# Kernel optimization log

Measured on AMD Instinct MI355X. Metric: run time of the kernel, lower is better.

Reference implementation:

```python
import jax, jax.numpy as jnp
import numpy as np

DIM = 768
HEADS = 12
HEAD_DIM = DIM // HEADS  # 64
THETA = 10000.0
B, S = 2, 2048


def rotate_half(x):
    # pairs-interleaved rotate: (x1, x2) -> (-x2, x1)
    xp = x.reshape(x.shape[:-1] + (-1, 2))
    x1, x2 = xp[..., 0], xp[..., 1]
    return jnp.stack((-x2, x1), axis=-1).reshape(x.shape)


def rope_freqs(seq_len, head_dim, dtype):
    inv = 1.0 / (THETA ** (jnp.arange(0, head_dim, 2, dtype=jnp.float32) / head_dim))
    pos = jnp.arange(seq_len, dtype=jnp.float32)
    f = pos[:, None] * inv[None, :]              # [S, head_dim//2]
    f = jnp.repeat(f, 2, axis=-1)                # [S, head_dim]
    return f.astype(dtype)


def apply_rotary(freqs, t):
    # freqs [S, D] broadcasts against t [B, H, S, D]
    return t * jnp.cos(freqs) + rotate_half(t) * jnp.sin(freqs)


def setup_inputs() -> dict:
    key = jax.random.key(0)
    k1, k2, k3 = jax.random.split(key, 3)
    x = jax.random.normal(k1, (B, S, DIM), dtype=jnp.float32)
    W_qkv = jax.random.normal(k2, (3 * DIM, DIM), dtype=jnp.float32) * 0.02
    W_proj = jax.random.normal(k3, (DIM, DIM), dtype=jnp.float32) * 0.02
    b_proj = jnp.zeros((DIM,), dtype=jnp.float32)
    return {"x": x, "W_qkv": W_qkv, "W_proj": W_proj, "b_proj": b_proj}


def reference(x, W_qkv, W_proj, b_proj):
    Bb, Ss, C = x.shape
    qkv = jnp.einsum('bsc,oc->bso', x, W_qkv)                    # [B,S,3C]
    qkv = qkv.reshape(Bb, Ss, 3, HEADS, HEAD_DIM)
    qkv = jnp.transpose(qkv, (2, 0, 3, 1, 4))                    # [3,B,H,S,D]
    q, k, v = qkv[0], qkv[1], qkv[2]
    freqs = rope_freqs(Ss, HEAD_DIM, x.dtype)
    q = apply_rotary(freqs, q)
    k = apply_rotary(freqs, k)
    scale = HEAD_DIM ** -0.5
    scores = jnp.einsum('bhqd,bhkd->bhqk', q, k) * scale         # [B,H,S,S]
    probs = jax.nn.softmax(scores, axis=-1)
    out = jnp.einsum('bhqk,bhkd->bhqd', probs, v)                # [B,H,S,D]
    out = jnp.transpose(out, (0, 2, 1, 3)).reshape(Bb, Ss, C)
    return jnp.einsum('bsc,oc->bso', out, W_proj) + b_proj
```

## Files before the change

### kernel.cpp

```cpp
#include <hip/hip_runtime.h>
#include <math.h>

#define Bq 2
#define Sq 2048
#define Cq 768
#define Hq 12
#define Dq 64

#define PANEL_SHORTS 98304
#define PANELS_X  32
#define PANELS_WQ 18
#define PANELS_WP 6

#define NROWS 49152
#define OPHALF 3145728
#define SPLIT_BLOCKS 2688
#define SM_SHIFT 8.0f

typedef _Float16 f16x8 __attribute__((ext_vector_type(8)));
typedef __fp16 fp16v2 __attribute__((ext_vector_type(2)));
typedef float f32x4 __attribute__((ext_vector_type(4)));
#define MFMA16F(a, b, c) __builtin_amdgcn_mfma_f32_16x16x32_f16(a, b, c, 0, 0, 0)

#define SCALEQ 0.18033688011112042f

static __device__ inline unsigned short f16bits(float x) {
    _Float16 h = (_Float16)x;
    return __builtin_bit_cast(unsigned short, h);
}
static __device__ inline unsigned int pk16(float a, float b) {
    fp16v2 h = __builtin_amdgcn_cvt_pkrtz(a, b);
    return __builtin_bit_cast(unsigned int, h);
}

static __device__ inline void gld_lds16(const unsigned short* g, unsigned short* l) {
    __builtin_amdgcn_global_load_lds(
        (const __attribute__((address_space(1))) unsigned int*)g,
        (__attribute__((address_space(3))) unsigned int*)l, 16, 0, 0);
}

__global__ __launch_bounds__(256) void split_kernel(
    const float* __restrict__ x, const float* __restrict__ wq,
    const float* __restrict__ wp,
    unsigned short* __restrict__ xs, unsigned short* __restrict__ wqs,
    unsigned short* __restrict__ wps,
    float* __restrict__ ctab, float* __restrict__ stab)
{
    if (blockIdx.x >= SPLIT_BLOCKS) {
        int idx = (blockIdx.x - SPLIT_BLOCKS) * 256 + threadIdx.x;
        int s = idx >> 5;
        int i = idx & 31;
        double f = (double)s * exp(-(double)i * 0.28782313662425573);
        ctab[idx] = (float)cos(f);
        stab[idx] = (float)sin(f);
        return;
    }
    const int cid  = blockIdx.x * 256 + threadIdx.x;
    const int panel = cid / 12288;
    const int pos8  = cid % 12288;
    const int step = pos8 >> 10;
    const int rem  = pos8 & 1023;
    const int J    = rem >> 6;
    const int lane = rem & 63;
    const int rowp = J * 8 + (lane >> 3);
    const int lc   = (lane & 7) ^ (rowp & 7);
    const int k    = step * 64 + lc * 8;
    const float* src; unsigned short* dst; int prow;
    if (panel < PANELS_X) {
        src = x;  dst = xs;  prow = panel;
    } else if (panel < PANELS_X + PANELS_WQ) {
        src = wq; dst = wqs; prow = panel - PANELS_X;
    } else {
        src = wp; dst = wps; prow = panel - PANELS_X - PANELS_WQ;
    }
    const int row = prow * 128 + rowp;
    float4 v0 = *(const float4*)(src + (size_t)row * Cq + k);
    float4 v1 = *(const float4*)(src + (size_t)row * Cq + k + 4);
    unsigned short o[8] = { f16bits(v0.x), f16bits(v0.y), f16bits(v0.z),
                            f16bits(v0.w), f16bits(v1.x), f16bits(v1.y),
                            f16bits(v1.z), f16bits(v1.w) };
    *(uint4*)&dst[(size_t)prow * PANEL_SHORTS + (size_t)pos8 * 8] = *(uint4*)o;
}

template <int MODE, int BM, int BN>
__global__ __launch_bounds__(256) void gemm_mfma_kernel(
    const unsigned short* __restrict__ Apr, const unsigned short* __restrict__ Bpr,
    const float* __restrict__ ctab, const float* __restrict__ stab,
    unsigned short* __restrict__ qp, unsigned short* __restrict__ kp,
    unsigned short* __restrict__ vp,
    float* __restrict__ out0, const float* __restrict__ bias)
{
    constexpr int MI  = BM / 32;
    constexpr int NI  = BN / 32;
    constexpr int WTM = BM / 2;
    constexpr int WTN = BN / 2;
    constexpr int BCH = BN / 8;
    constexpr int ACH = BM / 8;
    constexpr int CPW = (ACH + BCH) / 4;

    __shared__ unsigned short sA[BM * 64];
    __shared__ unsigned short sB[BN * 64];

    const int t    = threadIdx.x;
    const int w    = t >> 6;
    const int lane = t & 63;
    const int ml   = lane & 15;
    const int quad = lane >> 4;
    const int wm   = w >> 1;
    const int wn   = w & 1;

    const int mBase = blockIdx.y * BM;
    const int nBase = blockIdx.x * BN;

    const unsigned short* gpanA = Apr + (size_t)(mBase >> 7) * PANEL_SHORTS;
    const unsigned short* gpanB = Bpr + (size_t)(nBase >> 7) * PANEL_SHORTS;
    const int JbA = (mBase & 127) >> 3;
    const int JbB = (nBase & 127) >> 3;

    f32x4 acc[MI][NI];
    #pragma unroll
    for (int mi = 0; mi < MI; ++mi)
        #pragma unroll
        for (int ni = 0; ni < NI; ++ni)
            acc[mi][ni] = (f32x4){0.f, 0.f, 0.f, 0.f};

    for (int k0 = 0; k0 < 12; ++k0) {
        __syncthreads();
        #pragma unroll
        for (int cc = 0; cc < CPW; ++cc) {
            const int c = w * CPW + cc;
            if (c < BCH) {
                gld_lds16(gpanB + k0 * 8192 + (JbB + c) * 512 + lane * 8,
                          sB + c * 512);
            } else {
                const int a = c - BCH;
                gld_lds16(gpanA + k0 * 8192 + (JbA + a) * 512 + lane * 8,
                          sA + a * 512);
            }
        }
        __syncthreads();

        f16x8 aF[MI][2], bF[NI][2];
        #pragma unroll
        for (int mi = 0; mi < MI; ++mi) {
            const int row = wm * WTM + mi * 16 + ml;
            #pragma unroll
            for (int ks = 0; ks < 2; ++ks)
                aF[mi][ks] = *(const f16x8*)
                    &sA[row * 64 + (((ks * 4 + quad) ^ (row & 7)) << 3)];
        }
        #pragma unroll
        for (int ni = 0; ni < NI; ++ni) {
            const int row = wn * WTN + ni * 16 + ml;
            #pragma unroll
            for (int ks = 0; ks < 2; ++ks)
                bF[ni][ks] = *(const f16x8*)
                    &sB[row * 64 + (((ks * 4 + quad) ^ (row & 7)) << 3)];
        }
        #pragma unroll
        for (int mi = 0; mi < MI; ++mi)
            #pragma unroll
            for (int ni = 0; ni < NI; ++ni) {
                acc[mi][ni] = MFMA16F(aF[mi][0], bF[ni][0], acc[mi][ni]);
                acc[mi][ni] = MFMA16F(aF[mi][1], bF[ni][1], acc[mi][ni]);
            }
    }

    if (MODE == 0) {
        const int which = nBase / Cq;
        #pragma unroll
        for (int mi = 0; mi < MI; ++mi) {
            const int gm = mBase + wm * WTM + mi * 16 + quad * 4;
            const int bb = gm >> 11;
            const int s0 = gm & 2047;
            #pragma unroll
            for (int ni = 0; ni < NI; ++ni) {
                const int gn = nBase + wn * WTN + ni * 16 + ml;
                const int c  = gn - which * Cq;
                const int hh = c >> 6;
                const int dd = c & 63;
                const size_t hb = (size_t)(bb * Hq + hh);
                if (which < 2) {
                    #pragma unroll
                    for (int r = 0; r < 4; ++r) {
                        float val = acc[mi][ni][r];
                        float pv  = __shfl_xor(val, 1, 64);
                        const int fi = (s0 + r) * 32 + (dd >> 1);
                        float c0 = ctab[fi], sn = stab[fi];
                        float o = (dd & 1) ? (val * c0 + pv * sn)
                                           : (val * c0 - pv * sn);
                        if (which == 0) {
                            o *= SCALEQ;
                            qp[(hb * Sq + s0 + r) * 64 + dd] = f16bits(o);
                        } else {
                            const int ss = s0 + r, rr = ss & 63, kt2 = ss >> 6;
                            kp[(hb * 32 + kt2) * 4096 + rr * 64
                               + (((dd >> 3) ^ (rr & 7)) << 3) + (dd & 7)] = f16bits(o);
                        }
                    }
                } else {
                    unsigned short hv[4];
                    #pragma unroll
                    for (int r = 0; r < 4; ++r)
                        hv[r] = f16bits(acc[mi][ni][r]);
                    const int kt2 = s0 >> 6;
                    *(ushort4*)&vp[(hb * 32 + kt2) * 4096 + dd * 64
                        + ((((s0 & 63) >> 3) ^ (dd & 7)) << 3) + (s0 & 7)]
                        = *(ushort4*)hv;
                }
            }
        }
    } else {
        #pragma unroll
        for (int mi = 0; mi < MI; ++mi) {
            const int gm = mBase + wm * WTM + mi * 16 + quad * 4;
            #pragma unroll
            for (int ni = 0; ni < NI; ++ni) {
                const int gn = nBase + wn * WTN + ni * 16 + ml;
                const float bz = bias[gn];
                #pragma unroll
                for (int r = 0; r < 4; ++r)
                    out0[(size_t)(gm + r) * Cq + gn] = acc[mi][ni][r] + bz;
            }
        }
    }
}

__global__ __launch_bounds__(256, 6) void attn_mfma_kernel(
    const unsigned short* __restrict__ qp, const unsigned short* __restrict__ kp,
    const unsigned short* __restrict__ vp, unsigned short* __restrict__ op,
    float* __restrict__ lp)
{
    __shared__ __align__(16) unsigned short smem[12288];
    unsigned short* pb = smem + 8192;

    const int t    = threadIdx.x;
    const int w    = t >> 6;
    const int lane = t & 63;
    const int ml   = lane & 15;
    const int quad = lane >> 4;
    const int bi   = blockIdx.x;
    const int bh   = bi % 24;
    const int rest = bi / 24;
    const int qt   = rest >> 1;
    const int half = rest & 1;

    const bool isV = (w >= 2);
    const unsigned short* gsrc = isV ? vp : kp;
    const int Jb = (w & 1) * 4;
    const size_t gb = (size_t)bh * 131072;
    unsigned short* sdst = smem + (isV ? 4096 : 0);

    const size_t qrow = ((size_t)bh * Sq + qt * 64 + w * 16 + ml) * 64;
    f16x8 bQ[2];
    bQ[0] = *(const f16x8*)(qp + qrow + quad * 8);
    bQ[1] = *(const f16x8*)(qp + qrow + 32 + quad * 8);

    float l_st = 0.f;
    f32x4 O[4];
    #pragma unroll
    for (int ng = 0; ng < 4; ++ng) O[ng] = (f32x4){0.f, 0.f, 0.f, 0.f};

    unsigned short* pbl = pb + (w * 16 + ml) * 64;
    const int rsw = ml & 7;

    const unsigned short* k_s = smem;
    const unsigned short* v_s = smem + 4096;

    for (int kt16 = 0; kt16 < 16; ++kt16) {
        const int kt = half * 16 + kt16;
        __syncthreads();
        {
            const unsigned short* gt = gsrc + gb + (size_t)kt * 4096;
            #pragma unroll
            for (int j = 0; j < 4; ++j)
                gld_lds16(gt + (Jb + j) * 512 + lane * 8, sdst + (Jb + j) * 512);
        }
        __syncthreads();

        f32x4 S[4];
        #pragma unroll
        for (int ng = 0; ng < 4; ++ng) {
            const int row = ng * 16 + ml;
            f32x4 acc = (f32x4){-SM_SHIFT, -SM_SHIFT, -SM_SHIFT, -SM_SHIFT};
            #pragma unroll
            for (int ks = 0; ks < 2; ++ks) {
                f16x8 aK = *(const f16x8*)
                    &k_s[row * 64 + (((ks * 4 + quad) ^ (row & 7)) << 3)];
                acc = MFMA16F(aK, bQ[ks], acc);
            }
            S[ng] = acc;
        }

        #pragma unroll
        for (int ng = 0; ng < 4; ++ng) {
            float p0 = exp2f(S[ng][0]);
            float p1 = exp2f(S[ng][1]);
            float p2 = exp2f(S[ng][2]);
            float p3 = exp2f(S[ng][3]);
            l_st += (p0 + p1) + (p2 + p3);
            uint2 u;
            u.x = pk16(p0, p1);
            u.y = pk16(p2, p3);
            const int ch = ng * 2 + (quad >> 1);
            *(uint2*)&pbl[((ch ^ rsw) << 3) + (quad & 1) * 4] = u;
        }

        #pragma unroll
        for (int ks = 0; ks < 2; ++ks) {
            uint4 pu = *(const uint4*)&pbl[(((ks * 4 + quad) ^ rsw) << 3)];
            f16x8 bP = __builtin_bit_cast(f16x8, pu);
            #pragma unroll
            for (int ngd = 0; ngd < 4; ++ngd) {
                const int row = ngd * 16 + ml;
                f16x8 aV = *(const f16x8*)
                    &v_s[row * 64 + (((ks * 4 + quad) ^ (row & 7)) << 3)];
                O[ngd] = MFMA16F(aV, bP, O[ngd]);
            }
        }
    }

    l_st += __shfl_xor(l_st, 16, 64);
    l_st += __shfl_xor(l_st, 32, 64);

    const int srow = qt * 64 + w * 16 + ml;
    const size_t rowb = (size_t)half * NROWS + (size_t)bh * 2048 + srow;
    if (quad == 0) lp[rowb] = l_st;
    const float il = 1.0f / l_st;
    #pragma unroll
    for (int ngd = 0; ngd < 4; ++ngd) {
        unsigned short o4[4];
        #pragma unroll
        for (int r = 0; r < 4; ++r)
            o4[r] = f16bits(O[ngd][r] * il);
        *(ushort4*)&op[rowb * 64 + ngd * 16 + quad * 4] = *(ushort4*)o4;
    }
}

__global__ __launch_bounds__(256) void combine_kernel(
    const unsigned short* __restrict__ op, const float* __restrict__ lp,
    unsigned short* __restrict__ attns)
{
    const int g   = blockIdx.x * 256 + threadIdx.x;
    const int row = g >> 3;
    const int ch  = g & 7;
    const int bh  = row >> 11;
    const int s   = row & 2047;

    const float l1v = lp[row];
    const float l2v = lp[NROWS + row];
    const float inv = 1.0f / (l1v + l2v);
    const float c1 = l1v * inv, c2 = l2v * inv;

    f16x8 h1 = *(const f16x8*)(op + (size_t)row * 64 + ch * 8);
    f16x8 h2 = *(const f16x8*)(op + OPHALF + (size_t)row * 64 + ch * 8);
    unsigned short o[8];
    #pragma unroll
    for (int j = 0; j < 8; ++j)
        o[j] = f16bits(c1 * (float)h1[j] + c2 * (float)h2[j]);

    const int bb = bh / Hq, hh = bh % Hq;
    const int mrow = bb * 2048 + s;
    const int panel = mrow >> 7, r128 = mrow & 127;
    const size_t addr = (size_t)panel * PANEL_SHORTS
                      + (r128 >> 3) * 512 + (r128 & 7) * 64
                      + (size_t)hh * 8192
                      + ((ch ^ (r128 & 7)) << 3);
    *(uint4*)&attns[addr] = *(uint4*)o;
}

extern "C" void kernel_launch(void* const* d_in, const int* in_sizes, int n_in,
                              void* d_out, int out_size, void* d_ws, size_t ws_size,
                              hipStream_t stream) {
    const float* x     = (const float*)d_in[0];
    const float* Wqkv  = (const float*)d_in[1];
    const float* Wproj = (const float*)d_in[2];
    const float* bproj = (const float*)d_in[3];
    float* out = (float*)d_out;

    char* p = (char*)d_ws;
    unsigned short* xs    = (unsigned short*)p; p += (size_t)PANELS_X  * PANEL_SHORTS * 2;
    unsigned short* wqs   = (unsigned short*)p; p += (size_t)PANELS_WQ * PANEL_SHORTS * 2;
    unsigned short* wps   = (unsigned short*)p; p += (size_t)PANELS_WP * PANEL_SHORTS * 2;
    unsigned short* qp    = (unsigned short*)p; p += (size_t)24 * Sq * 64 * 2;
    unsigned short* kp    = (unsigned short*)p; p += (size_t)24 * 131072 * 2;
    unsigned short* vp    = (unsigned short*)p; p += (size_t)24 * 131072 * 2;
    unsigned short* attns = (unsigned short*)p; p += (size_t)PANELS_X * PANEL_SHORTS * 2;
    unsigned short* op    = (unsigned short*)p; p += (size_t)2 * OPHALF * 2;
    float* lp             = (float*)p;          p += (size_t)2 * NROWS * 4;
    float* ctab = (float*)p; p += (size_t)Sq * 32 * 4;
    float* stab = (float*)p; p += (size_t)Sq * 32 * 4;

    split_kernel<<<SPLIT_BLOCKS + 256, 256, 0, stream>>>(
        x, Wqkv, Wproj, xs, wqs, wps, ctab, stab);
    gemm_mfma_kernel<0, 64, 128><<<dim3(18, 64), 256, 0, stream>>>(
        xs, wqs, ctab, stab, qp, kp, vp, nullptr, nullptr);
    attn_mfma_kernel<<<dim3(24 * 64), 256, 0, stream>>>(qp, kp, vp, op, lp);
    combine_kernel<<<dim3(1536), 256, 0, stream>>>(op, lp, attns);
    gemm_mfma_kernel<1, 64, 64><<<dim3(12, 64), 256, 0, stream>>>(
        attns, wps, ctab, stab, nullptr, nullptr, nullptr, out, bproj);
}
```

Before: 176.7 us.

## Switch attention to 32x32 MFMA with 128-row query tiles and 4-way KV split

The attention kernel moves from 16x16x32 to 32x32x16 MFMA tiles, so each wave handles 32 query rows and a block covers 128 queries. The key range is split into four quarters instead of two, and the combine kernel now merges four partial outputs weighted by their partial sums. Larger tiles let each K/V tile loaded into LDS serve more queries and issue fewer MFMA instructions, while the extra split keeps the grid at the same block count. The costs are more partial-output traffic in the combine step, a larger LDS allocation, and a lower occupancy hint.

```diff
diff --git a/kernel.cpp b/kernel.cpp
--- a/kernel.cpp
+++ b/kernel.cpp
@@ -13,14 +13,16 @@
 #define PANELS_WP 6
 
 #define NROWS 49152
-#define OPHALF 3145728
+#define OPQTR 3145728
 #define SPLIT_BLOCKS 2688
 #define SM_SHIFT 8.0f
 
 typedef _Float16 f16x8 __attribute__((ext_vector_type(8)));
 typedef __fp16 fp16v2 __attribute__((ext_vector_type(2)));
 typedef float f32x4 __attribute__((ext_vector_type(4)));
+typedef float f32x16 __attribute__((ext_vector_type(16)));
 #define MFMA16F(a, b, c) __builtin_amdgcn_mfma_f32_16x16x32_f16(a, b, c, 0, 0, 0)
+#define MFMA32F(a, b, c) __builtin_amdgcn_mfma_f32_32x32x16_f16(a, b, c, 0, 0, 0)
 
 #define SCALEQ 0.18033688011112042f
 
@@ -226,49 +228,49 @@
     }
 }
 
-__global__ __launch_bounds__(256, 6) void attn_mfma_kernel(
+__global__ __launch_bounds__(256, 4) void attn_mfma_kernel(
     const unsigned short* __restrict__ qp, const unsigned short* __restrict__ kp,
     const unsigned short* __restrict__ vp, unsigned short* __restrict__ op,
     float* __restrict__ lp)
 {
-    __shared__ __align__(16) unsigned short smem[12288];
-    unsigned short* pb = smem + 8192;
+    __shared__ __align__(16) unsigned short smem[16384];
+    unsigned short* k_s = smem;
+    unsigned short* v_s = smem + 4096;
+    unsigned short* pb  = smem + 8192;
 
     const int t    = threadIdx.x;
     const int w    = t >> 6;
     const int lane = t & 63;
-    const int ml   = lane & 15;
-    const int quad = lane >> 4;
+    const int l31  = lane & 31;
+    const int hi   = lane >> 5;
     const int bi   = blockIdx.x;
     const int bh   = bi % 24;
     const int rest = bi / 24;
-    const int qt   = rest >> 1;
-    const int half = rest & 1;
+    const int qt   = rest >> 2;
+    const int qtr  = rest & 3;
 
     const bool isV = (w >= 2);
     const unsigned short* gsrc = isV ? vp : kp;
     const int Jb = (w & 1) * 4;
     const size_t gb = (size_t)bh * 131072;
-    unsigned short* sdst = smem + (isV ? 4096 : 0);
-
-    const size_t qrow = ((size_t)bh * Sq + qt * 64 + w * 16 + ml) * 64;
-    f16x8 bQ[2];
-    bQ[0] = *(const f16x8*)(qp + qrow + quad * 8);
-    bQ[1] = *(const f16x8*)(qp + qrow + 32 + quad * 8);
+    unsigned short* sdst = isV ? v_s : k_s;
+
+    const size_t qrow = ((size_t)bh * Sq + qt * 128 + w * 32 + l31) * 64;
+    f16x8 bQ[4];
+    #pragma unroll
+    for (int ks = 0; ks < 4; ++ks)
+        bQ[ks] = *(const f16x8*)(qp + qrow + ks * 16 + hi * 8);
 
     float l_st = 0.f;
-    f32x4 O[4];
+    f32x16 O0, O1;
     #pragma unroll
-    for (int ng = 0; ng < 4; ++ng) O[ng] = (f32x4){0.f, 0.f, 0.f, 0.f};
-
-    unsigned short* pbl = pb + (w * 16 + ml) * 64;
-    const int rsw = ml & 7;
-
-    const unsigned short* k_s = smem;
-    const unsigned short* v_s = smem + 4096;
-
-    for (int kt16 = 0; kt16 < 16; ++kt16) {
-        const int kt = half * 16 + kt16;
+    for (int e = 0; e < 16; ++e) { O0[e] = 0.f; O1[e] = 0.f; }
+
+    unsigned short* pbl = pb + (w * 32 + l31) * 64;
+    const int qsw = l31 & 7;
+
+    for (int kt8 = 0; kt8 < 8; ++kt8) {
+        const int kt = qtr * 8 + kt8;
         __syncthreads();
         {
             const unsigned short* gt = gsrc + gb + (size_t)kt * 4096;
@@ -278,62 +280,85 @@
         }
         __syncthreads();
 
-        f32x4 S[4];
-        #pragma unroll
-        for (int ng = 0; ng < 4; ++ng) {
-            const int row = ng * 16 + ml;
-            f32x4 acc = (f32x4){-SM_SHIFT, -SM_SHIFT, -SM_SHIFT, -SM_SHIFT};
-            #pragma unroll
-            for (int ks = 0; ks < 2; ++ks) {
+        f32x16 S0, S1;
+        #pragma unroll
+        for (int e = 0; e < 16; ++e) { S0[e] = -SM_SHIFT; S1[e] = -SM_SHIFT; }
+        #pragma unroll
+        for (int ks = 0; ks < 4; ++ks) {
+            const int g = ks * 2 + hi;
+            {
+                const int row = l31;
                 f16x8 aK = *(const f16x8*)
-                    &k_s[row * 64 + (((ks * 4 + quad) ^ (row & 7)) << 3)];
-                acc = MFMA16F(aK, bQ[ks], acc);
-            }
-            S[ng] = acc;
-        }
-
-        #pragma unroll
-        for (int ng = 0; ng < 4; ++ng) {
-            float p0 = exp2f(S[ng][0]);
-            float p1 = exp2f(S[ng][1]);
-            float p2 = exp2f(S[ng][2]);
-            float p3 = exp2f(S[ng][3]);
-            l_st += (p0 + p1) + (p2 + p3);
-            uint2 u;
-            u.x = pk16(p0, p1);
-            u.y = pk16(p2, p3);
-            const int ch = ng * 2 + (quad >> 1);
-            *(uint2*)&pbl[((ch ^ rsw) << 3) + (quad & 1) * 4] = u;
-        }
-
-        #pragma unroll
-        for (int ks = 0; ks < 2; ++ks) {
-            uint4 pu = *(const uint4*)&pbl[(((ks * 4 + quad) ^ rsw) << 3)];
+                    &k_s[row * 64 + ((g ^ (row & 7)) << 3)];
+                S0 = MFMA32F(aK, bQ[ks], S0);
+            }
+            {
+                const int row = 32 + l31;
+                f16x8 aK = *(const f16x8*)
+                    &k_s[row * 64 + ((g ^ (row & 7)) << 3)];
+                S1 = MFMA32F(aK, bQ[ks], S1);
+            }
+        }
+
+        #pragma unroll
+        for (int kt2 = 0; kt2 < 2; ++kt2) {
+            #pragma unroll
+            for (int g = 0; g < 4; ++g) {
+                float p0, p1, p2, p3;
+                if (kt2 == 0) {
+                    p0 = exp2f(S0[g * 4 + 0]); p1 = exp2f(S0[g * 4 + 1]);
+                    p2 = exp2f(S0[g * 4 + 2]); p3 = exp2f(S0[g * 4 + 3]);
+                } else {
+                    p0 = exp2f(S1[g * 4 + 0]); p1 = exp2f(S1[g * 4 + 1]);
+                    p2 = exp2f(S1[g * 4 + 2]); p3 = exp2f(S1[g * 4 + 3]);
+                }
+                l_st += (p0 + p1) + (p2 + p3);
+                uint2 u;
+                u.x = pk16(p0, p1);
+                u.y = pk16(p2, p3);
+                const int gran = kt2 * 4 + g;
+                *(uint2*)&pbl[((gran ^ qsw) << 3) + hi * 4] = u;
+            }
+        }
+
+        #pragma unroll
+        for (int kstep = 0; kstep < 4; ++kstep) {
+            const int gran = kstep * 2 + hi;
+            uint4 pu = *(const uint4*)&pbl[((gran ^ qsw) << 3)];
             f16x8 bP = __builtin_bit_cast(f16x8, pu);
-            #pragma unroll
-            for (int ngd = 0; ngd < 4; ++ngd) {
-                const int row = ngd * 16 + ml;
+            {
+                const int row = l31;
                 f16x8 aV = *(const f16x8*)
-                    &v_s[row * 64 + (((ks * 4 + quad) ^ (row & 7)) << 3)];
-                O[ngd] = MFMA16F(aV, bP, O[ngd]);
-            }
-        }
-    }
-
-    l_st += __shfl_xor(l_st, 16, 64);
+                    &v_s[row * 64 + ((gran ^ (row & 7)) << 3)];
+                O0 = MFMA32F(aV, bP, O0);
+            }
+            {
+                const int row = 32 + l31;
+                f16x8 aV = *(const f16x8*)
+                    &v_s[row * 64 + ((gran ^ (row & 7)) << 3)];
+                O1 = MFMA32F(aV, bP, O1);
+            }
+        }
+    }
+
     l_st += __shfl_xor(l_st, 32, 64);
 
-    const int srow = qt * 64 + w * 16 + ml;
-    const size_t rowb = (size_t)half * NROWS + (size_t)bh * 2048 + srow;
-    if (quad == 0) lp[rowb] = l_st;
+    const int srow = qt * 128 + w * 32 + l31;
+    const size_t rowb = (size_t)qtr * NROWS + (size_t)bh * 2048 + srow;
+    if (lane < 32) lp[rowb] = l_st;
     const float il = 1.0f / l_st;
     #pragma unroll
-    for (int ngd = 0; ngd < 4; ++ngd) {
-        unsigned short o4[4];
-        #pragma unroll
-        for (int r = 0; r < 4; ++r)
-            o4[r] = f16bits(O[ngd][r] * il);
-        *(ushort4*)&op[rowb * 64 + ngd * 16 + quad * 4] = *(ushort4*)o4;
+    for (int dt2 = 0; dt2 < 2; ++dt2) {
+        #pragma unroll
+        for (int g = 0; g < 4; ++g) {
+            unsigned short o4[4];
+            #pragma unroll
+            for (int r = 0; r < 4; ++r) {
+                float ov = dt2 ? O1[g * 4 + r] : O0[g * 4 + r];
+                o4[r] = f16bits(ov * il);
+            }
+            *(ushort4*)&op[rowb * 64 + dt2 * 32 + g * 8 + hi * 4] = *(ushort4*)o4;
+        }
     }
 }
 
@@ -347,17 +372,23 @@
     const int bh  = row >> 11;
     const int s   = row & 2047;
 
-    const float l1v = lp[row];
-    const float l2v = lp[NROWS + row];
-    const float inv = 1.0f / (l1v + l2v);
-    const float c1 = l1v * inv, c2 = l2v * inv;
-
-    f16x8 h1 = *(const f16x8*)(op + (size_t)row * 64 + ch * 8);
-    f16x8 h2 = *(const f16x8*)(op + OPHALF + (size_t)row * 64 + ch * 8);
+    const float w0 = lp[row];
+    const float w1 = lp[NROWS + row];
+    const float w2 = lp[2 * NROWS + row];
+    const float w3 = lp[3 * NROWS + row];
+    const float inv = 1.0f / (((w0 + w1) + (w2 + w3)));
+
+    f16x8 h0 = *(const f16x8*)(op + (size_t)row * 64 + ch * 8);
+    f16x8 h1 = *(const f16x8*)(op + (size_t)OPQTR + (size_t)row * 64 + ch * 8);
+    f16x8 h2 = *(const f16x8*)(op + (size_t)2 * OPQTR + (size_t)row * 64 + ch * 8);
+    f16x8 h3 = *(const f16x8*)(op + (size_t)3 * OPQTR + (size_t)row * 64 + ch * 8);
     unsigned short o[8];
     #pragma unroll
-    for (int j = 0; j < 8; ++j)
-        o[j] = f16bits(c1 * (float)h1[j] + c2 * (float)h2[j]);
+    for (int j = 0; j < 8; ++j) {
+        float v = (w0 * (float)h0[j] + w1 * (float)h1[j])
+                + (w2 * (float)h2[j] + w3 * (float)h3[j]);
+        o[j] = f16bits(v * inv);
+    }
 
     const int bb = bh / Hq, hh = bh % Hq;
     const int mrow = bb * 2048 + s;
@@ -386,8 +417,8 @@
     unsigned short* kp    = (unsigned short*)p; p += (size_t)24 * 131072 * 2;
     unsigned short* vp    = (unsigned short*)p; p += (size_t)24 * 131072 * 2;
     unsigned short* attns = (unsigned short*)p; p += (size_t)PANELS_X * PANEL_SHORTS * 2;
-    unsigned short* op    = (unsigned short*)p; p += (size_t)2 * OPHALF * 2;
-    float* lp             = (float*)p;          p += (size_t)2 * NROWS * 4;
+    unsigned short* op    = (unsigned short*)p; p += (size_t)4 * OPQTR * 2;
+    float* lp             = (float*)p;          p += (size_t)4 * NROWS * 4;
     float* ctab = (float*)p; p += (size_t)Sq * 32 * 4;
     float* stab = (float*)p; p += (size_t)Sq * 32 * 4;
 
```

Result: faster. 172.3 us (-2.5%).
